# Performance work log

Hardware: AMD Instinct MI355X
Metric: run time of the kernel (lower is better)

Reference implementation:

```python
import jax, jax.numpy as jnp
import numpy as np

N, E, G = 100000, 600000, 2000
CONV = [128, 256, 256, 256]
LIN = [256, 128, 1]
BN_EPS = 1e-5


def setup_inputs() -> dict:
    key = jax.random.key(0)
    ks = iter(jax.random.split(key, 64))
    inp = {}
    inp["x"] = jax.random.normal(next(ks), (N, CONV[0]), dtype=jnp.float32)
    inp["edge_index"] = jax.random.randint(next(ks), (2, E), 0, N)
    inp["batch"] = jnp.sort(jax.random.randint(next(ks), (N,), 0, G))

    def lin_w(k, i, o):
        return (jax.random.normal(k, (i, o), dtype=jnp.float32) / np.sqrt(i)).astype(jnp.float32)

    # 3 GINConv MLPs: Linear(in,out), BN(out), ReLU, Linear(out,out), ReLU
    for i in range(3):
        ci, co = CONV[i], CONV[i + 1]
        inp[f"c{i}_w1"] = lin_w(next(ks), ci, co)
        inp[f"c{i}_b1"] = jnp.zeros((co,), jnp.float32)
        inp[f"c{i}_g"] = jnp.ones((co,), jnp.float32)
        inp[f"c{i}_be"] = jnp.zeros((co,), jnp.float32)
        inp[f"c{i}_m"] = jax.random.normal(next(ks), (co,), dtype=jnp.float32) * 0.1
        inp[f"c{i}_v"] = jax.random.uniform(next(ks), (co,), minval=0.5, maxval=1.5, dtype=jnp.float32)
        inp[f"c{i}_w2"] = lin_w(next(ks), co, co)
        inp[f"c{i}_b2"] = jnp.zeros((co,), jnp.float32)
    # head: Linear(256,128) + BN(128) + ReLU, Linear(128,1)
    inp["l0_w"] = lin_w(next(ks), LIN[0], LIN[1])
    inp["l0_b"] = jnp.zeros((LIN[1],), jnp.float32)
    inp["l0_g"] = jnp.ones((LIN[1],), jnp.float32)
    inp["l0_be"] = jnp.zeros((LIN[1],), jnp.float32)
    inp["l0_m"] = jax.random.normal(next(ks), (LIN[1],), dtype=jnp.float32) * 0.1
    inp["l0_v"] = jax.random.uniform(next(ks), (LIN[1],), minval=0.5, maxval=1.5, dtype=jnp.float32)
    inp["l1_w"] = lin_w(next(ks), LIN[1], LIN[2])
    inp["l1_b"] = jnp.zeros((LIN[2],), jnp.float32)
    return inp


def _bn(h, g, be, m, v):
    return g * (h - m) * jax.lax.rsqrt(v + BN_EPS) + be


def _gin_conv(x, src, dst, w1, b1, g, be, m, v, w2, b2):
    # GINConv (eps=0): MLP(x + sum_{j in N(i)} x_j); messages x[src] aggregated at dst
    agg = jax.ops.segment_sum(x[src], dst, num_segments=x.shape[0])
    h = (x + agg) @ w1 + b1
    h = jax.nn.relu(_bn(h, g, be, m, v))
    return jax.nn.relu(h @ w2 + b2)


def reference(x, edge_index, batch,
              c0_w1, c0_b1, c0_g, c0_be, c0_m, c0_v, c0_w2, c0_b2,
              c1_w1, c1_b1, c1_g, c1_be, c1_m, c1_v, c1_w2, c1_b2,
              c2_w1, c2_b1, c2_g, c2_be, c2_m, c2_v, c2_w2, c2_b2,
              l0_w, l0_b, l0_g, l0_be, l0_m, l0_v, l1_w, l1_b):
    src, dst = edge_index[0], edge_index[1]
    conv_params = [
        (c0_w1, c0_b1, c0_g, c0_be, c0_m, c0_v, c0_w2, c0_b2),
        (c1_w1, c1_b1, c1_g, c1_be, c1_m, c1_v, c1_w2, c1_b2),
        (c2_w1, c2_b1, c2_g, c2_be, c2_m, c2_v, c2_w2, c2_b2),
    ]
    h = x
    for i, p in enumerate(conv_params):
        h = _gin_conv(h, src, dst, *p)
        if i < 2:
            h = jax.nn.relu(h)  # outer activation (no-op after ReLU, kept for fidelity)
    # global_add_pool over graphs
    h = jax.ops.segment_sum(h, batch, num_segments=G)  # [G, 256]
    h = h @ l0_w + l0_b
    h = _bn(h, l0_g, l0_be, l0_m, l0_v)
    h = jax.nn.relu(h)  # dropout is identity in eval mode
    return h @ l1_w + l1_b  # [G, 1]
```

## Files before the change

### kernel.cpp

```cpp
#include <hip/hip_runtime.h>
#include <hip/hip_bf16.h>

#define BN_EPS 1e-5f

typedef __attribute__((ext_vector_type(8))) short short8;
typedef __attribute__((ext_vector_type(4))) float f32x4;

__device__ __forceinline__ void gll16(const void* g, void* l) {
    __builtin_amdgcn_global_load_lds(
        (const __attribute__((address_space(1))) unsigned int*)g,
        (__attribute__((address_space(3))) unsigned int*)l, 16, 0, 0);
}

__device__ __forceinline__ unsigned pack_bf2(float a, float b) {
    __hip_bfloat16 ba = __float2bfloat16(a);
    __hip_bfloat16 bb = __float2bfloat16(b);
    return (unsigned)(*(unsigned short*)&ba) | ((unsigned)(*(unsigned short*)&bb) << 16);
}

__global__ void hist_kernel(const int* __restrict__ dst, int* __restrict__ off, int E) {
    int e = blockIdx.x * blockDim.x + threadIdx.x;
    if (e < E) atomicAdd(&off[dst[e] + 1], 1);
}

__global__ __launch_bounds__(256) void scan1_kernel(int* __restrict__ data,
                                                    int* __restrict__ sums, int n) {
    __shared__ int sh[256];
    const int t = threadIdx.x;
    const int idx = blockIdx.x * 1024 + t * 4;
    int v[4];
    int s = 0;
#pragma unroll
    for (int j = 0; j < 4; ++j) {
        int x = (idx + j < n) ? data[idx + j] : 0;
        s += x;
        v[j] = s;
    }
    sh[t] = s;
    __syncthreads();
    for (int o = 1; o < 256; o <<= 1) {
        int x = (t >= o) ? sh[t - o] : 0;
        __syncthreads();
        sh[t] += x;
        __syncthreads();
    }
    const int prev = sh[t] - s;
#pragma unroll
    for (int j = 0; j < 4; ++j) {
        if (idx + j < n) data[idx + j] = v[j] + prev;
    }
    if (t == 255) sums[blockIdx.x] = sh[255];
}

__global__ __launch_bounds__(256) void scan2_kernel(int* __restrict__ sums, int nb) {
    __shared__ int sh[256];
    const int t = threadIdx.x;
    sh[t] = (t < nb) ? sums[t] : 0;
    __syncthreads();
    for (int o = 1; o < 256; o <<= 1) {
        int x = (t >= o) ? sh[t - o] : 0;
        __syncthreads();
        sh[t] += x;
        __syncthreads();
    }
    if (t < nb) sums[t] = sh[t];
}

__global__ void scan3_kernel(int* __restrict__ data, const int* __restrict__ sums,
                             int* __restrict__ cursor, int n, int N) {
    int i = blockIdx.x * blockDim.x + threadIdx.x;
    if (i >= n) return;
    int b = i >> 10;
    int v = data[i];
    if (b > 0) { v += sums[b - 1]; data[i] = v; }
    if (i < N) cursor[i] = v;
}

__global__ void fill_kernel(const int* __restrict__ src, const int* __restrict__ dst,
                            int* __restrict__ cursor, int* __restrict__ sorted_src, int E) {
    int e = blockIdx.x * blockDim.x + threadIdx.x;
    if (e >= E) return;
    int p = atomicAdd(&cursor[dst[e]], 1);
    sorted_src[p] = src[e];
}

__global__ void cvt_x_kernel(const float* __restrict__ x, __hip_bfloat16* __restrict__ xb,
                             int N, int total ) {
    int i = blockIdx.x * blockDim.x + threadIdx.x;
    if (i >= total) return;
    int n = i >> 7;
    float v = (n < N) ? x[i] : 0.f;
    xb[i] = __float2bfloat16(v);
}

__global__ void wt_all_kernel(const float* __restrict__ w0, const float* __restrict__ w1,
                              const float* __restrict__ w2, const float* __restrict__ w3,
                              const float* __restrict__ w4, const float* __restrict__ w5,
                              __hip_bfloat16* __restrict__ o0, __hip_bfloat16* __restrict__ o1,
                              __hip_bfloat16* __restrict__ o2, __hip_bfloat16* __restrict__ o3,
                              __hip_bfloat16* __restrict__ o4, __hip_bfloat16* __restrict__ o5) {
    int i = blockIdx.x * blockDim.x + threadIdx.x;
    const int S0 = 256 * 128, S = 256 * 256;
    if (i < S0) {
        int m = i / 128, k = i - m * 128;
        o0[i] = __float2bfloat16(w0[k * 256 + m]);
        return;
    }
    i -= S0;
    int mi = i / S, j = i - mi * S;
    if (mi >= 5) return;
    int m = j >> 8, k = j & 255;
    const float* Wp; __hip_bfloat16* Op;
    switch (mi) {
        case 0: Wp = w1; Op = o1; break;
        case 1: Wp = w2; Op = o2; break;
        case 2: Wp = w3; Op = o3; break;
        case 3: Wp = w4; Op = o4; break;
        default: Wp = w5; Op = o5; break;
    }
    Op[j] = __float2bfloat16(Wp[k * 256 + m]);
}

__global__ void prep_ss_kernel(
    const float* __restrict__ g0, const float* __restrict__ be0, const float* __restrict__ m0,
    const float* __restrict__ v0, const float* __restrict__ b10, const float* __restrict__ b20,
    const float* __restrict__ g1, const float* __restrict__ be1, const float* __restrict__ m1,
    const float* __restrict__ v1, const float* __restrict__ b11, const float* __restrict__ b21,
    const float* __restrict__ g2, const float* __restrict__ be2, const float* __restrict__ m2,
    const float* __restrict__ v2, const float* __restrict__ b12, const float* __restrict__ b22,
    float* __restrict__ ss) {
    const int layer = blockIdx.x;
    const int c = threadIdx.x;
    const float *g, *be, *m, *v, *b1, *b2;
    switch (layer) {
        case 0: g = g0; be = be0; m = m0; v = v0; b1 = b10; b2 = b20; break;
        case 1: g = g1; be = be1; m = m1; v = v1; b1 = b11; b2 = b21; break;
        default: g = g2; be = be2; m = m2; v = v2; b1 = b12; b2 = b22; break;
    }
    float r = rsqrtf(v[c] + BN_EPS);
    float s = g[c] * r;
    ss[(2 * layer) * 512 + c] = s;
    ss[(2 * layer) * 512 + 256 + c] = (b1[c] - m[c]) * s + be[c];
    ss[(2 * layer + 1) * 512 + c] = 1.f;
    ss[(2 * layer + 1) * 512 + 256 + c] = b2[c];
}

template <int C>
__global__ __launch_bounds__(256) void agg_fused(const __hip_bfloat16* __restrict__ h,
                                                 const int* __restrict__ off,
                                                 const int* __restrict__ ssrc,
                                                 __hip_bfloat16* __restrict__ out, int N) {
    constexpr int L = C / 8;
    int t = blockIdx.x * blockDim.x + threadIdx.x;
    int n = t / L;
    if (n >= N) return;
    int c8 = t - n * L;
    const uint4* hp = (const uint4*)h;

    float acc[8];
    {
        uint4 sv = hp[(size_t)n * L + c8];
        const unsigned u[4] = {sv.x, sv.y, sv.z, sv.w};
#pragma unroll
        for (int j = 0; j < 4; ++j) {
            acc[2 * j]     = __uint_as_float(u[j] << 16);
            acc[2 * j + 1] = __uint_as_float(u[j] & 0xffff0000u);
        }
    }
    const int e0 = off[n], e1 = off[n + 1];
    int e = e0;
    for (; e + 2 <= e1; e += 2) {
        int s0 = ssrc[e], s1 = ssrc[e + 1];
        uint4 a = hp[(size_t)s0 * L + c8];
        uint4 b = hp[(size_t)s1 * L + c8];
        const unsigned ua[4] = {a.x, a.y, a.z, a.w};
        const unsigned ub[4] = {b.x, b.y, b.z, b.w};
#pragma unroll
        for (int j = 0; j < 4; ++j) {
            acc[2 * j]     += __uint_as_float(ua[j] << 16);
            acc[2 * j + 1] += __uint_as_float(ua[j] & 0xffff0000u);
            acc[2 * j]     += __uint_as_float(ub[j] << 16);
            acc[2 * j + 1] += __uint_as_float(ub[j] & 0xffff0000u);
        }
    }
    if (e < e1) {
        int s0 = ssrc[e];
        uint4 a = hp[(size_t)s0 * L + c8];
        const unsigned ua[4] = {a.x, a.y, a.z, a.w};
#pragma unroll
        for (int j = 0; j < 4; ++j) {
            acc[2 * j]     += __uint_as_float(ua[j] << 16);
            acc[2 * j + 1] += __uint_as_float(ua[j] & 0xffff0000u);
        }
    }
    unsigned o[4];
#pragma unroll
    for (int j = 0; j < 4; ++j) o[j] = pack_bf2(acc[2 * j], acc[2 * j + 1]);
    ((uint4*)out)[(size_t)n * L + c8] = make_uint4(o[0], o[1], o[2], o[3]);
}

template <int K1>
__global__ __launch_bounds__(512, 4) void mlp_fused(
    const __hip_bfloat16* __restrict__ A,
    const __hip_bfloat16* __restrict__ W1t,
    const __hip_bfloat16* __restrict__ W2t,
    const float* __restrict__ ss1, const float* __restrict__ ss2,
    __hip_bfloat16* __restrict__ C) {
    __shared__ __align__(16) char bufAT[32 * 1024];
    __shared__ __align__(16) char bufW[32 * 1024];

    const int tid = threadIdx.x;
    const int l   = tid & 63;
    const int w   = tid >> 6;
    const int wr  = w >> 2;
    const int wc  = w & 3;
    const size_t row0 = (size_t)blockIdx.x * 64;

    constexpr int ROWB = K1 * 2;
    constexpr int NT1  = K1 / 64;
    const int lswz = (l & 7) << 4;

    {
        const char* Ab = (const char*)(A + row0 * K1);
        constexpr int NIA = 64 * ROWB / 1024;
        constexpr int RPI = 1024 / ROWB;
#pragma unroll
        for (int i = w; i < NIA; i += 8) {
            int row = i * RPI + (l * 16) / ROWB;
            int byt = ((l * 16) % ROWB) ^ ((row & 7) << 4);
            gll16(Ab + (size_t)row * ROWB + byt, bufAT + i * 1024);
        }
    }
    auto stageW = [&](const __hip_bfloat16* Wsrc, int Krow2, int t) {
#pragma unroll
        for (int i = w; i < 32; i += 8) {
            int c = i * 8 + (l >> 3);
            int byt = ((l & 7) * 16) ^ ((l >> 3) << 4);
            gll16((const char*)Wsrc + (size_t)c * Krow2 + t * 128 + byt, bufW + i * 1024);
        }
    };
    stageW(W1t, ROWB, 0);
    asm volatile("s_waitcnt vmcnt(0)" ::: "memory");
    __syncthreads();

    f32x4 acc1[4][2] = {};
#pragma unroll
    for (int t = 0; t < NT1; ++t) {
#pragma unroll
        for (int k0 = 0; k0 < 2; ++k0) {
            short8 wf[4], af[2];
            const int wbyt = (k0 * 64 + (l >> 4) * 16) ^ lswz;
            const int abyt = (t * 128 + k0 * 64 + (l >> 4) * 16) ^ lswz;
#pragma unroll
            for (int i = 0; i < 4; ++i)
                wf[i] = *(const short8*)(bufW + (wc * 64 + i * 16 + (l & 15)) * 128 + wbyt);
#pragma unroll
            for (int i = 0; i < 2; ++i)
                af[i] = *(const short8*)(bufAT + (wr * 32 + i * 16 + (l & 15)) * ROWB + abyt);
#pragma unroll
            for (int mi = 0; mi < 4; ++mi)
#pragma unroll
                for (int nj = 0; nj < 2; ++nj)
                    acc1[mi][nj] = __builtin_amdgcn_mfma_f32_16x16x32_bf16(
                        wf[mi], af[nj], acc1[mi][nj], 0, 0, 0);
        }
        __syncthreads();
        if (t + 1 < NT1) {
            stageW(W1t, ROWB, t + 1);
            asm volatile("s_waitcnt vmcnt(0)" ::: "memory");
            __syncthreads();
        }
    }

    stageW(W2t, 512, 0);
#pragma unroll
    for (int mi = 0; mi < 4; ++mi) {
        const int m0 = wc * 64 + mi * 16 + (l >> 4) * 4;
        const float4 s4 = *(const float4*)(ss1 + m0);
        const float4 h4 = *(const float4*)(ss1 + 256 + m0);
        const int byt = (m0 * 2) ^ lswz;
#pragma unroll
        for (int nj = 0; nj < 2; ++nj) {
            const int n = wr * 32 + nj * 16 + (l & 15);
            const float v0 = fmaxf(acc1[mi][nj][0] * s4.x + h4.x, 0.f);
            const float v1 = fmaxf(acc1[mi][nj][1] * s4.y + h4.y, 0.f);
            const float v2 = fmaxf(acc1[mi][nj][2] * s4.z + h4.z, 0.f);
            const float v3 = fmaxf(acc1[mi][nj][3] * s4.w + h4.w, 0.f);
            *(uint2*)(bufAT + n * 512 + byt) = make_uint2(pack_bf2(v0, v1), pack_bf2(v2, v3));
        }
    }
    asm volatile("s_waitcnt vmcnt(0)" ::: "memory");
    __syncthreads();

    f32x4 acc2[4][2] = {};
#pragma unroll
    for (int s = 0; s < 4; ++s) {
#pragma unroll
        for (int k0 = 0; k0 < 2; ++k0) {
            short8 wf[4], tf[2];
            const int wbyt = (k0 * 64 + (l >> 4) * 16) ^ lswz;
            const int tbyt = (s * 128 + k0 * 64 + (l >> 4) * 16) ^ lswz;
#pragma unroll
            for (int i = 0; i < 4; ++i)
                wf[i] = *(const short8*)(bufW + (wc * 64 + i * 16 + (l & 15)) * 128 + wbyt);
#pragma unroll
            for (int i = 0; i < 2; ++i)
                tf[i] = *(const short8*)(bufAT + (wr * 32 + i * 16 + (l & 15)) * 512 + tbyt);
#pragma unroll
            for (int ni = 0; ni < 4; ++ni)
#pragma unroll
                for (int mj = 0; mj < 2; ++mj)
                    acc2[ni][mj] = __builtin_amdgcn_mfma_f32_16x16x32_bf16(
                        wf[ni], tf[mj], acc2[ni][mj], 0, 0, 0);
        }
        __syncthreads();
        if (s < 3) {
            stageW(W2t, 512, s + 1);
            asm volatile("s_waitcnt vmcnt(0)" ::: "memory");
            __syncthreads();
        }
    }

#pragma unroll
    for (int ni = 0; ni < 4; ++ni) {
        const int c0 = wc * 64 + ni * 16 + (l >> 4) * 4;
        const float4 s4 = *(const float4*)(ss2 + c0);
        const float4 h4 = *(const float4*)(ss2 + 256 + c0);
        const int byt = (c0 * 2) ^ lswz;
#pragma unroll
        for (int mj = 0; mj < 2; ++mj) {
            const int n = wr * 32 + mj * 16 + (l & 15);
            const float v0 = fmaxf(acc2[ni][mj][0] * s4.x + h4.x, 0.f);
            const float v1 = fmaxf(acc2[ni][mj][1] * s4.y + h4.y, 0.f);
            const float v2 = fmaxf(acc2[ni][mj][2] * s4.z + h4.z, 0.f);
            const float v3 = fmaxf(acc2[ni][mj][3] * s4.w + h4.w, 0.f);
            *(uint2*)(bufAT + n * 512 + byt) = make_uint2(pack_bf2(v0, v1), pack_bf2(v2, v3));
        }
    }
    __syncthreads();

    {
        char* Cb = (char*)C + row0 * 512;
#pragma unroll
        for (int q = tid; q < 2048; q += 512) {
            const int n = q >> 5;
            const int slot = (q & 31) * 16;
            uint4 v = *(const uint4*)(bufAT + n * 512 + (slot ^ ((n & 7) << 4)));
            *(uint4*)(Cb + q * 16) = v;
        }
    }
}

__device__ __forceinline__ int lower_bound_dev(const int* __restrict__ a, int n, int key) {
    int lo = 0, hi = n;
    while (lo < hi) {
        int mid = (lo + hi) >> 1;
        if (a[mid] < key) lo = mid + 1; else hi = mid;
    }
    return lo;
}

__global__ __launch_bounds__(256) void pool_seg_kernel(const __hip_bfloat16* __restrict__ h,
                                                       const int* __restrict__ batch,
                                                       float* __restrict__ pooled, int N) {
    __shared__ int seg[2];
    const int g = blockIdx.x;
    if (threadIdx.x == 0) seg[0] = lower_bound_dev(batch, N, g);
    if (threadIdx.x == 1) seg[1] = lower_bound_dev(batch, N, g + 1);
    __syncthreads();
    const int c = threadIdx.x;
    float acc = 0.f;
    for (int n = seg[0]; n < seg[1]; ++n) acc += __bfloat162float(h[(size_t)n * 256 + c]);
    pooled[(size_t)g * 256 + c] = acc;
}

__global__ __launch_bounds__(128) void head_kernel(
    const float* __restrict__ pooled,
    const float* __restrict__ w0, const float* __restrict__ b0,
    const float* __restrict__ g, const float* __restrict__ be,
    const float* __restrict__ m, const float* __restrict__ v,
    const float* __restrict__ w1, const float* __restrict__ b1,
    float* __restrict__ out) {
    __shared__ float row[256];
    __shared__ float red[128];
    const int gid = blockIdx.x;
    const int j = threadIdx.x;

    row[j]       = pooled[(size_t)gid * 256 + j];
    row[j + 128] = pooled[(size_t)gid * 256 + 128 + j];
    __syncthreads();

    float acc = b0[j];
#pragma unroll 8
    for (int k = 0; k < 256; ++k) acc += row[k] * w0[k * 128 + j];

    float h = g[j] * (acc - m[j]) * rsqrtf(v[j] + BN_EPS) + be[j];
    h = fmaxf(h, 0.f) * w1[j];
    red[j] = h;
    __syncthreads();
    for (int s = 64; s > 0; s >>= 1) {
        if (j < s) red[j] += red[j + s];
        __syncthreads();
    }
    if (j == 0) out[gid] = red[0] + b1[0];
}

extern "C" void kernel_launch(void* const* d_in, const int* in_sizes, int n_in,
                              void* d_out, int out_size, void* d_ws, size_t ws_size,
                              hipStream_t stream) {
    const float* x    = (const float*)d_in[0];
    const int* eidx   = (const int*)d_in[1];
    const int* batch  = (const int*)d_in[2];

    const int N = in_sizes[0] / 128;
    const int E = in_sizes[1] / 2;
    const int G = out_size;

    const int* src = eidx;
    const int* dst = eidx + E;

    const float* cw1[3]; const float* cb1[3]; const float* cg[3]; const float* cbe[3];
    const float* cm[3];  const float* cv[3];  const float* cw2[3]; const float* cb2[3];
    for (int i = 0; i < 3; ++i) {
        int b = 3 + i * 8;
        cw1[i] = (const float*)d_in[b + 0];
        cb1[i] = (const float*)d_in[b + 1];
        cg[i]  = (const float*)d_in[b + 2];
        cbe[i] = (const float*)d_in[b + 3];
        cm[i]  = (const float*)d_in[b + 4];
        cv[i]  = (const float*)d_in[b + 5];
        cw2[i] = (const float*)d_in[b + 6];
        cb2[i] = (const float*)d_in[b + 7];
    }
    const float* l0_w  = (const float*)d_in[27];
    const float* l0_b  = (const float*)d_in[28];
    const float* l0_g  = (const float*)d_in[29];
    const float* l0_be = (const float*)d_in[30];
    const float* l0_m  = (const float*)d_in[31];
    const float* l0_v  = (const float*)d_in[32];
    const float* l1_w  = (const float*)d_in[33];
    const float* l1_b  = (const float*)d_in[34];

    float* outp = (float*)d_out;

    const int nrb  = (N + 127) / 128;
    const int Npad = nrb * 128;
    const int nrb64 = Npad / 64;
    const size_t SB = (size_t)Npad * 256 * 2;
    const size_t XB = (size_t)Npad * 128 * 2;
    const size_t PB = (size_t)G * 256 * 4;
    const size_t WTB = (size_t)256 * 256 * 2;

    char* ws = (char*)d_ws;
    size_t o = 0;
    __hip_bfloat16* U  = (__hip_bfloat16*)(ws + o); o += SB;
    __hip_bfloat16* V  = (__hip_bfloat16*)(ws + o); o += SB;
    __hip_bfloat16* xb = (__hip_bfloat16*)(ws + o); o += XB;
    float* pooled      = (float*)(ws + o);       o += PB;
    __hip_bfloat16* wt[6];
    for (int i = 0; i < 6; ++i) { wt[i] = (__hip_bfloat16*)(ws + o); o += WTB; }
    float* ss          = (float*)(ws + o);       o += 6 * 512 * 4;
    int* csr_off    = (int*)(ws + o); o += (size_t)(N + 1) * 4;
    int* cursor     = (int*)(ws + o); o += (size_t)N * 4;
    int* sorted_src = (int*)(ws + o); o += (size_t)E * 4;
    int* sums       = (int*)(ws + o); o += 256 * 4;
    if (ws_size < o) return;

    const dim3 blk(256);

    {
        int total = Npad * 128;
        cvt_x_kernel<<<(total + 255) / 256, blk, 0, stream>>>(x, xb, N, total);
    }
    {
        int total = 256 * 128 + 5 * 256 * 256;
        wt_all_kernel<<<(total + 255) / 256, blk, 0, stream>>>(
            cw1[0], cw2[0], cw1[1], cw2[1], cw1[2], cw2[2],
            wt[0], wt[1], wt[2], wt[3], wt[4], wt[5]);
    }
    prep_ss_kernel<<<3, blk, 0, stream>>>(
        cg[0], cbe[0], cm[0], cv[0], cb1[0], cb2[0],
        cg[1], cbe[1], cm[1], cv[1], cb1[1], cb2[1],
        cg[2], cbe[2], cm[2], cv[2], cb1[2], cb2[2], ss);

    {
        const int n_off = N + 1;
        hipMemsetAsync(csr_off, 0, (size_t)n_off * sizeof(int), stream);
        hist_kernel<<<(E + 255) / 256, blk, 0, stream>>>(dst, csr_off, E);
        const int nb = (n_off + 1023) / 1024;
        scan1_kernel<<<nb, blk, 0, stream>>>(csr_off, sums, n_off);
        scan2_kernel<<<1, blk, 0, stream>>>(sums, nb);
        scan3_kernel<<<(n_off + 255) / 256, blk, 0, stream>>>(csr_off, sums, cursor, n_off, N);
        fill_kernel<<<(E + 255) / 256, blk, 0, stream>>>(src, dst, cursor, sorted_src, E);
    }

    auto SS = [&](int i) { return ss + i * 512; };

    {
        int total = N * 16;
        agg_fused<128><<<(total + 255) / 256, blk, 0, stream>>>(xb, csr_off, sorted_src, U, N);
    }
    mlp_fused<128><<<nrb64, dim3(512), 0, stream>>>(U, wt[0], wt[1], SS(0), SS(1), V);

    {
        int total = N * 32;
        agg_fused<256><<<(total + 255) / 256, blk, 0, stream>>>(V, csr_off, sorted_src, U, N);
    }
    mlp_fused<256><<<nrb64, dim3(512), 0, stream>>>(U, wt[2], wt[3], SS(2), SS(3), U);

    {
        int total = N * 32;
        agg_fused<256><<<(total + 255) / 256, blk, 0, stream>>>(U, csr_off, sorted_src, V, N);
    }
    mlp_fused<256><<<nrb64, dim3(512), 0, stream>>>(V, wt[4], wt[5], SS(4), SS(5), V);

    pool_seg_kernel<<<G, blk, 0, stream>>>(V, batch, pooled, N);
    head_kernel<<<G, dim3(128), 0, stream>>>(pooled, l0_w, l0_b, l0_g, l0_be, l0_m, l0_v,
                                             l1_w, l1_b, outp);
}
```

Measured before the change: 405.5 us.

## Load MLP weights directly into registers per wave and vectorize x conversion

The fused MLP kernel no longer stages weight tiles through shared memory. Each wave now owns 32 output channels, reads its weight fragments straight from global memory (expected to be L2-resident), and covers all 64 rows of the block. This drops the weight LDS buffer and most of the barriers and waits, halving shared memory so more blocks can be resident per CU. In exchange, each wave issues uncoalesced per-lane global weight loads and loses the reuse that shared staging gave. Separately, the x fp32-to-bf16 conversion now handles four elements per thread with vector loads and stores.

```diff
diff --git a/kernel.cpp b/kernel.cpp
--- a/kernel.cpp
+++ b/kernel.cpp
@@ -85,12 +85,17 @@
 }
 
 __global__ void cvt_x_kernel(const float* __restrict__ x, __hip_bfloat16* __restrict__ xb,
-                             int N, int total ) {
+                             int N, int total4 ) {
     int i = blockIdx.x * blockDim.x + threadIdx.x;
-    if (i >= total) return;
-    int n = i >> 7;
-    float v = (n < N) ? x[i] : 0.f;
-    xb[i] = __float2bfloat16(v);
+    if (i >= total4) return;
+    int n = i >> 5;
+    unsigned lo = 0, hi = 0;
+    if (n < N) {
+        const float4 v = ((const float4*)x)[i];
+        lo = pack_bf2(v.x, v.y);
+        hi = pack_bf2(v.z, v.w);
+    }
+    ((uint2*)xb)[i] = make_uint2(lo, hi);
 }
 
 __global__ void wt_all_kernel(const float* __restrict__ w0, const float* __restrict__ w1,
@@ -206,18 +211,17 @@
     const __hip_bfloat16* __restrict__ W2t,
     const float* __restrict__ ss1, const float* __restrict__ ss2,
     __hip_bfloat16* __restrict__ C) {
-    __shared__ __align__(16) char bufAT[32 * 1024];
-    __shared__ __align__(16) char bufW[32 * 1024];
+    __shared__ __align__(16) char bufT[32 * 1024];
 
     const int tid = threadIdx.x;
     const int l   = tid & 63;
     const int w   = tid >> 6;
-    const int wr  = w >> 2;
-    const int wc  = w & 3;
     const size_t row0 = (size_t)blockIdx.x * 64;
 
     constexpr int ROWB = K1 * 2;
-    constexpr int NT1  = K1 / 64;
+    constexpr int NT1  = K1 / 32;
+    const int l15  = l & 15;
+    const int kg   = l >> 4;
     const int lswz = (l & 7) << 4;
 
     {
@@ -228,113 +232,88 @@
         for (int i = w; i < NIA; i += 8) {
             int row = i * RPI + (l * 16) / ROWB;
             int byt = ((l * 16) % ROWB) ^ ((row & 7) << 4);
-            gll16(Ab + (size_t)row * ROWB + byt, bufAT + i * 1024);
-        }
-    }
-    auto stageW = [&](const __hip_bfloat16* Wsrc, int Krow2, int t) {
-#pragma unroll
-        for (int i = w; i < 32; i += 8) {
-            int c = i * 8 + (l >> 3);
-            int byt = ((l & 7) * 16) ^ ((l >> 3) << 4);
-            gll16((const char*)Wsrc + (size_t)c * Krow2 + t * 128 + byt, bufW + i * 1024);
-        }
-    };
-    stageW(W1t, ROWB, 0);
+            gll16(Ab + (size_t)row * ROWB + byt, bufT + i * 1024);
+        }
+    }
     asm volatile("s_waitcnt vmcnt(0)" ::: "memory");
     __syncthreads();
 
-    f32x4 acc1[4][2] = {};
-#pragma unroll
-    for (int t = 0; t < NT1; ++t) {
-#pragma unroll
-        for (int k0 = 0; k0 < 2; ++k0) {
-            short8 wf[4], af[2];
-            const int wbyt = (k0 * 64 + (l >> 4) * 16) ^ lswz;
-            const int abyt = (t * 128 + k0 * 64 + (l >> 4) * 16) ^ lswz;
-#pragma unroll
-            for (int i = 0; i < 4; ++i)
-                wf[i] = *(const short8*)(bufW + (wc * 64 + i * 16 + (l & 15)) * 128 + wbyt);
-#pragma unroll
-            for (int i = 0; i < 2; ++i)
-                af[i] = *(const short8*)(bufAT + (wr * 32 + i * 16 + (l & 15)) * ROWB + abyt);
-#pragma unroll
-            for (int mi = 0; mi < 4; ++mi)
-#pragma unroll
-                for (int nj = 0; nj < 2; ++nj)
-                    acc1[mi][nj] = __builtin_amdgcn_mfma_f32_16x16x32_bf16(
-                        wf[mi], af[nj], acc1[mi][nj], 0, 0, 0);
-        }
-        __syncthreads();
-        if (t + 1 < NT1) {
-            stageW(W1t, ROWB, t + 1);
-            asm volatile("s_waitcnt vmcnt(0)" ::: "memory");
-            __syncthreads();
-        }
-    }
-
-    stageW(W2t, 512, 0);
-#pragma unroll
-    for (int mi = 0; mi < 4; ++mi) {
-        const int m0 = wc * 64 + mi * 16 + (l >> 4) * 4;
+    f32x4 acc1[2][4] = {};
+    {
+        const char* wp0 = (const char*)W1t + (size_t)(w * 32 + l15) * ROWB + kg * 16;
+        const char* wp1 = wp0 + 16 * ROWB;
+#pragma unroll
+        for (int t = 0; t < NT1; ++t) {
+            const short8 wf0 = *(const short8*)(wp0 + t * 64);
+            const short8 wf1 = *(const short8*)(wp1 + t * 64);
+            short8 af[4];
+            const int abyt = (t * 64 + kg * 16) ^ lswz;
+#pragma unroll
+            for (int j = 0; j < 4; ++j)
+                af[j] = *(const short8*)(bufT + (j * 16 + l15) * ROWB + abyt);
+#pragma unroll
+            for (int j = 0; j < 4; ++j) {
+                acc1[0][j] = __builtin_amdgcn_mfma_f32_16x16x32_bf16(wf0, af[j], acc1[0][j], 0, 0, 0);
+                acc1[1][j] = __builtin_amdgcn_mfma_f32_16x16x32_bf16(wf1, af[j], acc1[1][j], 0, 0, 0);
+            }
+        }
+    }
+    __syncthreads();
+
+#pragma unroll
+    for (int i = 0; i < 2; ++i) {
+        const int m0 = w * 32 + i * 16 + kg * 4;
         const float4 s4 = *(const float4*)(ss1 + m0);
         const float4 h4 = *(const float4*)(ss1 + 256 + m0);
         const int byt = (m0 * 2) ^ lswz;
 #pragma unroll
-        for (int nj = 0; nj < 2; ++nj) {
-            const int n = wr * 32 + nj * 16 + (l & 15);
-            const float v0 = fmaxf(acc1[mi][nj][0] * s4.x + h4.x, 0.f);
-            const float v1 = fmaxf(acc1[mi][nj][1] * s4.y + h4.y, 0.f);
-            const float v2 = fmaxf(acc1[mi][nj][2] * s4.z + h4.z, 0.f);
-            const float v3 = fmaxf(acc1[mi][nj][3] * s4.w + h4.w, 0.f);
-            *(uint2*)(bufAT + n * 512 + byt) = make_uint2(pack_bf2(v0, v1), pack_bf2(v2, v3));
-        }
-    }
-    asm volatile("s_waitcnt vmcnt(0)" ::: "memory");
-    __syncthreads();
-
-    f32x4 acc2[4][2] = {};
-#pragma unroll
-    for (int s = 0; s < 4; ++s) {
-#pragma unroll
-        for (int k0 = 0; k0 < 2; ++k0) {
-            short8 wf[4], tf[2];
-            const int wbyt = (k0 * 64 + (l >> 4) * 16) ^ lswz;
-            const int tbyt = (s * 128 + k0 * 64 + (l >> 4) * 16) ^ lswz;
-#pragma unroll
-            for (int i = 0; i < 4; ++i)
-                wf[i] = *(const short8*)(bufW + (wc * 64 + i * 16 + (l & 15)) * 128 + wbyt);
-#pragma unroll
-            for (int i = 0; i < 2; ++i)
-                tf[i] = *(const short8*)(bufAT + (wr * 32 + i * 16 + (l & 15)) * 512 + tbyt);
-#pragma unroll
-            for (int ni = 0; ni < 4; ++ni)
-#pragma unroll
-                for (int mj = 0; mj < 2; ++mj)
-                    acc2[ni][mj] = __builtin_amdgcn_mfma_f32_16x16x32_bf16(
-                        wf[ni], tf[mj], acc2[ni][mj], 0, 0, 0);
-        }
-        __syncthreads();
-        if (s < 3) {
-            stageW(W2t, 512, s + 1);
-            asm volatile("s_waitcnt vmcnt(0)" ::: "memory");
-            __syncthreads();
-        }
-    }
-
-#pragma unroll
-    for (int ni = 0; ni < 4; ++ni) {
-        const int c0 = wc * 64 + ni * 16 + (l >> 4) * 4;
+        for (int j = 0; j < 4; ++j) {
+            const int n = j * 16 + l15;
+            const float v0 = fmaxf(acc1[i][j][0] * s4.x + h4.x, 0.f);
+            const float v1 = fmaxf(acc1[i][j][1] * s4.y + h4.y, 0.f);
+            const float v2 = fmaxf(acc1[i][j][2] * s4.z + h4.z, 0.f);
+            const float v3 = fmaxf(acc1[i][j][3] * s4.w + h4.w, 0.f);
+            *(uint2*)(bufT + n * 512 + byt) = make_uint2(pack_bf2(v0, v1), pack_bf2(v2, v3));
+        }
+    }
+    __syncthreads();
+
+    f32x4 acc2[2][4] = {};
+    {
+        const char* wp0 = (const char*)W2t + (size_t)(w * 32 + l15) * 512 + kg * 16;
+        const char* wp1 = wp0 + 16 * 512;
+#pragma unroll
+        for (int t = 0; t < 8; ++t) {
+            const short8 wf0 = *(const short8*)(wp0 + t * 64);
+            const short8 wf1 = *(const short8*)(wp1 + t * 64);
+            short8 tf[4];
+            const int tbyt = (t * 64 + kg * 16) ^ lswz;
+#pragma unroll
+            for (int j = 0; j < 4; ++j)
+                tf[j] = *(const short8*)(bufT + (j * 16 + l15) * 512 + tbyt);
+#pragma unroll
+            for (int j = 0; j < 4; ++j) {
+                acc2[0][j] = __builtin_amdgcn_mfma_f32_16x16x32_bf16(wf0, tf[j], acc2[0][j], 0, 0, 0);
+                acc2[1][j] = __builtin_amdgcn_mfma_f32_16x16x32_bf16(wf1, tf[j], acc2[1][j], 0, 0, 0);
+            }
+        }
+    }
+    __syncthreads();
+
+#pragma unroll
+    for (int i = 0; i < 2; ++i) {
+        const int c0 = w * 32 + i * 16 + kg * 4;
         const float4 s4 = *(const float4*)(ss2 + c0);
         const float4 h4 = *(const float4*)(ss2 + 256 + c0);
         const int byt = (c0 * 2) ^ lswz;
 #pragma unroll
-        for (int mj = 0; mj < 2; ++mj) {
-            const int n = wr * 32 + mj * 16 + (l & 15);
-            const float v0 = fmaxf(acc2[ni][mj][0] * s4.x + h4.x, 0.f);
-            const float v1 = fmaxf(acc2[ni][mj][1] * s4.y + h4.y, 0.f);
-            const float v2 = fmaxf(acc2[ni][mj][2] * s4.z + h4.z, 0.f);
-            const float v3 = fmaxf(acc2[ni][mj][3] * s4.w + h4.w, 0.f);
-            *(uint2*)(bufAT + n * 512 + byt) = make_uint2(pack_bf2(v0, v1), pack_bf2(v2, v3));
+        for (int j = 0; j < 4; ++j) {
+            const int n = j * 16 + l15;
+            const float v0 = fmaxf(acc2[i][j][0] * s4.x + h4.x, 0.f);
+            const float v1 = fmaxf(acc2[i][j][1] * s4.y + h4.y, 0.f);
+            const float v2 = fmaxf(acc2[i][j][2] * s4.z + h4.z, 0.f);
+            const float v3 = fmaxf(acc2[i][j][3] * s4.w + h4.w, 0.f);
+            *(uint2*)(bufT + n * 512 + byt) = make_uint2(pack_bf2(v0, v1), pack_bf2(v2, v3));
         }
     }
     __syncthreads();
@@ -345,7 +324,7 @@
         for (int q = tid; q < 2048; q += 512) {
             const int n = q >> 5;
             const int slot = (q & 31) * 16;
-            uint4 v = *(const uint4*)(bufAT + n * 512 + (slot ^ ((n & 7) << 4)));
+            uint4 v = *(const uint4*)(bufT + n * 512 + (slot ^ ((n & 7) << 4)));
             *(uint4*)(Cb + q * 16) = v;
         }
     }
@@ -469,8 +448,8 @@
     const dim3 blk(256);
 
     {
-        int total = Npad * 128;
-        cvt_x_kernel<<<(total + 255) / 256, blk, 0, stream>>>(x, xb, N, total);
+        int total4 = Npad * 128 / 4;
+        cvt_x_kernel<<<(total4 + 255) / 256, blk, 0, stream>>>(x, xb, N, total4);
     }
     {
         int total = 256 * 128 + 5 * 256 * 256;
```

Measured after the change: 460.2 us. 13.5% more time.
